# Kernel tuning notes

Measured on AMD Instinct MI355X. Metric: run time of the kernel, lower is better.

## Reference

```python
import jax, jax.numpy as jnp
import numpy as np

RESID = 1024
HEADS = 16
HEAD_DIM = 64


def setup_inputs() -> dict:
    key = jax.random.key(0)
    ks = jax.random.split(key, 6)
    B, S = 2, 2048
    residual_stream = jax.random.normal(ks[0], (B, S, RESID), dtype=jnp.float32)
    # per-head qkv linear params, stacked over heads: [H, resid, 3*head_dim]
    W_qkv = jax.random.normal(ks[1], (HEADS, RESID, 3 * HEAD_DIM), dtype=jnp.float32) * (1.0 / np.sqrt(RESID))
    b_qkv = jax.random.normal(ks[2], (HEADS, 3 * HEAD_DIM), dtype=jnp.float32) * 0.01
    # output projection resid -> resid
    W_o = jax.random.normal(ks[3], (RESID, RESID), dtype=jnp.float32) * (1.0 / np.sqrt(RESID))
    b_o = jax.random.normal(ks[4], (RESID,), dtype=jnp.float32) * 0.01
    return {"residual_stream": residual_stream, "W_qkv": W_qkv, "b_qkv": b_qkv, "W_o": W_o, "b_o": b_o}


def reference(residual_stream, W_qkv, b_qkv, W_o, b_o):
    # qkv per head: [B, H, S, 3*D]
    qkv = jnp.einsum('bsr,hrd->bhsd', residual_stream, W_qkv) + b_qkv[None, :, None, :]
    q = qkv[..., :HEAD_DIM]
    k = qkv[..., HEAD_DIM:2 * HEAD_DIM]
    v = qkv[..., 2 * HEAD_DIM:]
    # NOTE: original has no causal mask; softmax over full key axis
    scores = jnp.einsum('bhsd,bhtd->bhst', q, k) / jnp.sqrt(jnp.float32(HEAD_DIM))
    attn = jax.nn.softmax(scores, axis=-1)
    out = jnp.einsum('bhst,bhtd->bhsd', attn, v)  # [B, H, S, D]
    B, H, S, D = out.shape
    out = out.transpose(0, 2, 1, 3).reshape(B, S, H * D)  # concat heads -> [B, S, resid]
    return out @ W_o + b_o
```

## Files before the change

kernel.cpp:

```cpp
#include <hip/hip_runtime.h>
#include <hip/hip_bf16.h>

#define B_ 2
#define S_ 2048
#define H_ 16
#define HD 64
#define R_ 1024
#define N_ (B_*S_)

typedef unsigned short ushort_t;
typedef short bf16x8 __attribute__((ext_vector_type(8)));
typedef float f32x4 __attribute__((ext_vector_type(4)));
typedef float f32x16 __attribute__((ext_vector_type(16)));

#define MFMA(a,b,c) __builtin_amdgcn_mfma_f32_16x16x32_bf16(a,b,c,0,0,0)
#define MFMA32(a,b,c) __builtin_amdgcn_mfma_f32_32x32x16_bf16(a,b,c,0,0,0)
#define GLD16(g,l) __builtin_amdgcn_global_load_lds( \
    (const __attribute__((address_space(1))) void*)(g), \
    (__attribute__((address_space(3))) void*)(l), 16, 0, 0)

__device__ __forceinline__ unsigned short f2bf(float f) {
  unsigned int u = __builtin_bit_cast(unsigned int, f);
  u += 0x7fffu + ((u >> 16) & 1u);
  return (unsigned short)(u >> 16);
}

__device__ __forceinline__ unsigned int cvtpk(float lo, float hi) {
  unsigned int r;
  asm("v_cvt_pk_bf16_f32 %0, %1, %2" : "=v"(r) : "v"(lo), "v"(hi));
  return r;
}

__device__ __forceinline__ void plswap(unsigned int &a, unsigned int &b) {
  asm volatile("v_permlane32_swap_b32 %0, %1" : "+v"(a), "+v"(b));
}

#if __has_builtin(__builtin_amdgcn_exp2f)
__device__ __forceinline__ float EXP2(float x) { return __builtin_amdgcn_exp2f(x); }
#else
__device__ __forceinline__ float EXP2(float x) {
  float r; asm("v_exp_f32 %0, %1" : "=v"(r) : "v"(x)); return r;
}
#endif

#if __has_builtin(__builtin_amdgcn_rcpf)
__device__ __forceinline__ float RCP(float x) { return __builtin_amdgcn_rcpf(x); }
#else
__device__ __forceinline__ float RCP(float x) { return 1.0f / x; }
#endif

__device__ __forceinline__ bf16x8 ld8(const ushort_t* p) {
  return *(const bf16x8*)p;
}

__device__ __forceinline__ void transpose_tile(const float* __restrict__ in,
                                               ushort_t* __restrict__ out,
                                               int rows, int cols, int rt, int ct,
                                               float (*t)[65], int tid) {
  const int r0 = rt * 64, c0 = ct * 64;
  const int tx = tid & 63, ty = tid >> 6;
  #pragma unroll
  for (int i = 0; i < 16; i++) {
    int r = ty * 16 + i;
    t[r][tx] = in[(size_t)(r0 + r) * cols + c0 + tx];
  }
  __syncthreads();
  #pragma unroll
  for (int i = 0; i < 16; i++) {
    int c = ty * 16 + i;
    out[(size_t)(c0 + c) * rows + r0 + tx] = f2bf(t[tx][c]);
  }
}

__global__ __launch_bounds__(256) void k_prep(
    const float* __restrict__ x, ushort_t* __restrict__ xb,
    const float* __restrict__ Wqkv, ushort_t* __restrict__ WT,
    const float* __restrict__ Wo, ushort_t* __restrict__ WoT) {
  __shared__ float t[64][65];
  const int bid = blockIdx.x, tid = threadIdx.x;
  if (bid < 4096) {
    int i = bid * 256 + tid;
    float4 v = ((const float4*)x)[i];
    ushort4 o;
    o.x = f2bf(v.x); o.y = f2bf(v.y); o.z = f2bf(v.z); o.w = f2bf(v.w);
    ((ushort4*)xb)[i] = o;
  } else if (bid < 4096 + 768) {
    int tt = bid - 4096;
    int z = tt / 48, rem = tt % 48;
    transpose_tile(Wqkv + (size_t)z * 1024 * 192, WT + (size_t)z * 192 * 1024,
                   1024, 192, rem % 16, rem / 16, t, tid);
  } else {
    int tt = bid - (4096 + 768);
    transpose_tile(Wo, WoT, 1024, 1024, tt % 16, tt / 16, t, tid);
  }
}

__global__ __launch_bounds__(256, 2) void k_qkv(
    const ushort_t* __restrict__ Xb, const ushort_t* __restrict__ WT,
    const float* __restrict__ bqkv,
    ushort_t* __restrict__ Q, ushort_t* __restrict__ K, ushort_t* __restrict__ Vt) {
  __shared__ ushort_t lA[2][128 * 32];
  __shared__ ushort_t lB[2][192 * 32];
  const int m0 = blockIdx.x * 128;
  const int h  = blockIdx.y;
  const int tid = threadIdx.x;
  const int w = tid >> 6, l = tid & 63;
  const int lr = l & 15, lg = l >> 4;
  const int wr = w >> 1, wc = w & 1;

  const ushort_t* Asrc = Xb + (size_t)m0 * R_;
  const ushort_t* Bsrc = WT + (size_t)h * 192 * R_;
  const int arow = l >> 2;
  const int acol = (l & 3) * 8;

  f32x4 acc[4][6];
  const f32x4 fz = {0.f, 0.f, 0.f, 0.f};
  #pragma unroll
  for (int m = 0; m < 4; m++)
    #pragma unroll
    for (int n = 0; n < 6; n++) acc[m][n] = fz;

  auto stage = [&](int buf, int kt) {
    const int k0 = kt * 32;
    #pragma unroll
    for (int i = 0; i < 2; i++) {
      int chunk = w + 4 * i;
      GLD16(Asrc + (size_t)(chunk * 16 + arow) * R_ + k0 + acol, &lA[buf][chunk * 512]);
    }
    #pragma unroll
    for (int i = 0; i < 3; i++) {
      int chunk = w + 4 * i;
      GLD16(Bsrc + (size_t)(chunk * 16 + arow) * R_ + k0 + acol, &lB[buf][chunk * 512]);
    }
  };

  stage(0, 0);
  asm volatile("s_waitcnt vmcnt(0)" ::: "memory");
  __syncthreads();

  int cur = 0;
  for (int kt = 0; kt < 32; ++kt) {
    if (kt < 31) stage(cur ^ 1, kt + 1);
    bf16x8 af[4], bfr[6];
    #pragma unroll
    for (int m = 0; m < 4; m++)
      af[m] = ld8(&lA[cur][(wr * 64 + m * 16 + lr) * 32 + lg * 8]);
    #pragma unroll
    for (int n = 0; n < 6; n++)
      bfr[n] = ld8(&lB[cur][(wc * 96 + n * 16 + lr) * 32 + lg * 8]);
    __builtin_amdgcn_s_setprio(1);
    #pragma unroll
    for (int m = 0; m < 4; m++)
      #pragma unroll
      for (int n = 0; n < 6; n++)
        acc[m][n] = MFMA(af[m], bfr[n], acc[m][n]);
    __builtin_amdgcn_s_setprio(0);
    asm volatile("s_waitcnt vmcnt(0)" ::: "memory");
    __syncthreads();
    cur ^= 1;
  }

  #pragma unroll
  for (int n = 0; n < 6; n++) {
    const int col = wc * 96 + n * 16 + lr;
    const float bias = bqkv[h * 192 + col];
    #pragma unroll
    for (int m = 0; m < 4; m++) {
      const int rb = m0 + wr * 64 + m * 16 + lg * 4;
      #pragma unroll
      for (int r = 0; r < 4; r++) {
        float v = acc[m][n][r] + bias;
        int srow = rb + r;
        int b = srow >> 11, s = srow & 2047;
        size_t bh = (size_t)b * H_ + h;
        if (col < 64) {
          Q[(bh * S_ + s) * HD + col] = f2bf(v * 0.1803368801111137f);
        } else if (col < 128) {
          int d = col - 64;
          K[(bh * S_ + s) * HD + d] = f2bf(v);
        } else {
          int d = col - 128;
          Vt[(bh * HD + d) * S_ + s] = f2bf(v);
        }
      }
    }
  }
}

__global__ __launch_bounds__(256, 2) void k_attn(
    const ushort_t* __restrict__ Q, const ushort_t* __restrict__ K,
    const ushort_t* __restrict__ Vt, ushort_t* __restrict__ AO) {
  __shared__ ushort_t sK[3][64 * 64];
  __shared__ ushort_t sV[3][64 * 64];
  const int qt = blockIdx.x;
  const int bh = blockIdx.y;
  const int b = bh >> 4, h = bh & 15;
  const int tid = threadIdx.x, w = tid >> 6, l = tid & 63;
  const int lq = l & 31, hi = l >> 5;

  const ushort_t* Qb = Q + (size_t)bh * S_ * HD;
  const ushort_t* Kb = K + (size_t)bh * S_ * HD;
  const ushort_t* Vb = Vt + (size_t)bh * HD * S_;

  bf16x8 qf[4];
  {
    int qrow = qt * 128 + 32 * w + lq;
    #pragma unroll
    for (int kd = 0; kd < 4; kd++)
      qf[kd] = ld8(&Qb[(size_t)qrow * HD + kd * 16 + hi * 8]);
  }

  const int sr = l >> 3;
  const int scol = l & 7;
  const int r0l = w * 16 + sr;
  const ushort_t* kp = Kb + (size_t)r0l * HD + scol * 8;
  const ushort_t* vp = Vb + (size_t)r0l * S_ + scol * 8;
  bf16x8 kreg0, kreg1, vreg0, vreg1;
  int tnext = 0;
  auto issue = [&]() {
    if (tnext < 32) {
      kreg0 = ld8(kp); kreg1 = ld8(kp + 8 * HD);
      vreg0 = ld8(vp); vreg1 = ld8(vp + 8 * S_);
      kp += 64 * HD; vp += 64;
    }
    ++tnext;
  };
  const int coff0 = r0l * 64 + ((scol ^ sr) * 8);
  const int coff1 = coff0 + 8 * 64;
  auto commit = [&](ushort_t* bK, ushort_t* bV) {
    *(bf16x8*)&bK[coff0] = kreg0; *(bf16x8*)&bK[coff1] = kreg1;
    *(bf16x8*)&bV[coff0] = vreg0; *(bf16x8*)&bV[coff1] = vreg1;
  };

  const f32x16 fz16 = {0};
  const bf16x8 onesv = {0x3F80, 0x3F80, 0x3F80, 0x3F80, 0x3F80, 0x3F80, 0x3F80, 0x3F80};
  f32x16 oacc0 = fz16, oacc1 = fz16, ssv = fz16;

  const int c = hi ^ (lq & 7);

  auto QK = [&](const ushort_t* bK, f32x16& s0, f32x16& s1) {
    f32x16 a0 = fz16, a1 = fz16;
    __builtin_amdgcn_s_setprio(1);
    #pragma unroll
    for (int kd = 0; kd < 4; kd++) {
      const int sl = ((kd * 2) ^ c) * 8;
      bf16x8 ka0 = ld8(&bK[lq * 64 + sl]);
      bf16x8 ka1 = ld8(&bK[(32 + lq) * 64 + sl]);
      a0 = MFMA32(ka0, qf[kd], a0);
      a1 = MFMA32(ka1, qf[kd], a1);
    }
    __builtin_amdgcn_s_setprio(0);
    s0 = a0; s1 = a1;
  };

  auto SMPV = [&](const ushort_t* bV, f32x16 s0, f32x16 s1) {
    #pragma unroll
    for (int n = 0; n < 2; n++) {
      const f32x16 scv = n ? s1 : s0;
      float e[16];
      #pragma unroll
      for (int r = 0; r < 16; r++) e[r] = EXP2(scv[r]);
      #pragma unroll
      for (int sl2 = 0; sl2 < 2; sl2++) {
        unsigned int X  = cvtpk(e[8 * sl2 + 0], e[8 * sl2 + 1]);
        unsigned int Y  = cvtpk(e[8 * sl2 + 2], e[8 * sl2 + 3]);
        unsigned int X2 = cvtpk(e[8 * sl2 + 4], e[8 * sl2 + 5]);
        unsigned int Y2 = cvtpk(e[8 * sl2 + 6], e[8 * sl2 + 7]);
        plswap(X, X2);
        plswap(Y, Y2);
        int4 wv = {(int)X, (int)Y, (int)X2, (int)Y2};
        bf16x8 pa = __builtin_bit_cast(bf16x8, wv);
        const int ks = n * 2 + sl2;
        const int sl3 = ((ks * 2) ^ c) * 8;
        __builtin_amdgcn_s_setprio(1);
        ssv = MFMA32(pa, onesv, ssv);
        {
          bf16x8 vb0 = ld8(&bV[lq * 64 + sl3]);
          bf16x8 vb1 = ld8(&bV[(32 + lq) * 64 + sl3]);
          oacc0 = MFMA32(pa, vb0, oacc0);
          oacc1 = MFMA32(pa, vb1, oacc1);
        }
        __builtin_amdgcn_s_setprio(0);
      }
    }
  };

  f32x16 scA0, scA1, scB0, scB1;
  issue();
  commit(sK[0], sV[0]);
  issue();
  __syncthreads();
  QK(sK[0], scA0, scA1);
  commit(sK[1], sV[1]);
  __syncthreads();
  issue();

#define ABODY(C, N, O, SI0, SI1, SO0, SO1) \
    QK(sK[N], SO0, SO1); \
    SMPV(sV[C], SI0, SI1); \
    commit(sK[O], sV[O]); \
    issue(); \
    __syncthreads();

  for (int kt = 0; kt < 30; kt += 6) {
    ABODY(0, 1, 2, scA0, scA1, scB0, scB1)
    ABODY(1, 2, 0, scB0, scB1, scA0, scA1)
    ABODY(2, 0, 1, scA0, scA1, scB0, scB1)
    ABODY(0, 1, 2, scB0, scB1, scA0, scA1)
    ABODY(1, 2, 0, scA0, scA1, scB0, scB1)
    ABODY(2, 0, 1, scB0, scB1, scA0, scA1)
  }
#undef ABODY

  QK(sK[1], scB0, scB1);
  SMPV(sV[0], scA0, scA1);
  SMPV(sV[1], scB0, scB1);

  #pragma unroll
  for (int reg = 0; reg < 16; reg++) {
    float inv = RCP(ssv[reg]);
    int qloc = (reg & 3) + 8 * (reg >> 2) + 4 * hi;
    int s = qt * 128 + 32 * w + qloc;
    AO[(size_t)(b * S_ + s) * R_ + h * HD + lq] = f2bf(oacc0[reg] * inv);
    AO[(size_t)(b * S_ + s) * R_ + h * HD + 32 + lq] = f2bf(oacc1[reg] * inv);
  }
}

__global__ __launch_bounds__(256, 2) void k_out(
    const ushort_t* __restrict__ AO, const ushort_t* __restrict__ WoT,
    const float* __restrict__ bo, float* __restrict__ out) {
  __shared__ ushort_t lA[2][128 * 32];
  __shared__ ushort_t lB[2][128 * 32];
  const int m0 = blockIdx.x * 128, n0 = blockIdx.y * 128;
  const int tid = threadIdx.x, w = tid >> 6, l = tid & 63;
  const int lr = l & 15, lg = l >> 4;
  const int wr = w >> 1, wc = w & 1;
  const ushort_t* Asrc = AO + (size_t)m0 * R_;
  const ushort_t* Bsrc = WoT + (size_t)n0 * R_;
  const int arow = l >> 2, acol = (l & 3) * 8;

  f32x4 acc[4][4];
  const f32x4 fz = {0.f, 0.f, 0.f, 0.f};
  #pragma unroll
  for (int m = 0; m < 4; m++)
    #pragma unroll
    for (int n = 0; n < 4; n++) acc[m][n] = fz;

  auto stage = [&](int buf, int kt) {
    const int k0 = kt * 32;
    #pragma unroll
    for (int i = 0; i < 2; i++) {
      int chunk = w + 4 * i;
      GLD16(Asrc + (size_t)(chunk * 16 + arow) * R_ + k0 + acol, &lA[buf][chunk * 512]);
      GLD16(Bsrc + (size_t)(chunk * 16 + arow) * R_ + k0 + acol, &lB[buf][chunk * 512]);
    }
  };

  stage(0, 0);
  asm volatile("s_waitcnt vmcnt(0)" ::: "memory");
  __syncthreads();

  int cur = 0;
  for (int kt = 0; kt < 32; ++kt) {
    if (kt < 31) stage(cur ^ 1, kt + 1);
    bf16x8 af[4], bfr[4];
    #pragma unroll
    for (int m = 0; m < 4; m++)
      af[m] = ld8(&lA[cur][(wr * 64 + m * 16 + lr) * 32 + lg * 8]);
    #pragma unroll
    for (int n = 0; n < 4; n++)
      bfr[n] = ld8(&lB[cur][(wc * 64 + n * 16 + lr) * 32 + lg * 8]);
    __builtin_amdgcn_s_setprio(1);
    #pragma unroll
    for (int m = 0; m < 4; m++)
      #pragma unroll
      for (int n = 0; n < 4; n++)
        acc[m][n] = MFMA(af[m], bfr[n], acc[m][n]);
    __builtin_amdgcn_s_setprio(0);
    asm volatile("s_waitcnt vmcnt(0)" ::: "memory");
    __syncthreads();
    cur ^= 1;
  }

  #pragma unroll
  for (int n = 0; n < 4; n++) {
    const int col = n0 + wc * 64 + n * 16 + lr;
    const float bias = bo[col];
    #pragma unroll
    for (int m = 0; m < 4; m++) {
      const int row = m0 + wr * 64 + m * 16 + lg * 4;
      #pragma unroll
      for (int r = 0; r < 4; r++)
        out[(size_t)(row + r) * R_ + col] = acc[m][n][r] + bias;
    }
  }
}

extern "C" void kernel_launch(void* const* d_in, const int* in_sizes, int n_in,
                              void* d_out, int out_size, void* d_ws, size_t ws_size,
                              hipStream_t stream) {
  const float* resid = (const float*)d_in[0];
  const float* Wqkv  = (const float*)d_in[1];
  const float* bqkv  = (const float*)d_in[2];
  const float* Wo    = (const float*)d_in[3];
  const float* bo    = (const float*)d_in[4];
  float* out = (float*)d_out;

  ushort_t* Xb  = (ushort_t*)d_ws;
  ushort_t* WT  = Xb  + (size_t)N_ * R_;
  ushort_t* WoT = WT  + (size_t)H_ * 192 * R_;
  ushort_t* Qd  = WoT + (size_t)R_ * R_;
  ushort_t* Kd  = Qd  + (size_t)B_ * H_ * S_ * HD;
  ushort_t* Vtd = Kd  + (size_t)B_ * H_ * S_ * HD;
  ushort_t* AOd = Vtd + (size_t)B_ * H_ * S_ * HD;

  k_prep<<<dim3(4096 + 768 + 256), dim3(256), 0, stream>>>(resid, Xb, Wqkv, WT, Wo, WoT);
  k_qkv<<<dim3(32, 16), dim3(256), 0, stream>>>(Xb, WT, bqkv, Qd, Kd, Vtd);
  k_attn<<<dim3(16, 32), dim3(256), 0, stream>>>(Qd, Kd, Vtd, AOd);
  k_out<<<dim3(32, 8), dim3(256), 0, stream>>>(AOd, WoT, bo, out);
}
```

Before: 120.2 us.

## Retile QKV GEMM to 128x128 across heads and XOR-swizzle LDS in GEMMs

```diff
diff --git a/kernel.cpp b/kernel.cpp
--- a/kernel.cpp
+++ b/kernel.cpp
@@ -95,30 +95,30 @@
   }
 }
 
-__global__ __launch_bounds__(256, 2) void k_qkv(
+__global__ __launch_bounds__(256, 3) void k_qkv(
     const ushort_t* __restrict__ Xb, const ushort_t* __restrict__ WT,
     const float* __restrict__ bqkv,
     ushort_t* __restrict__ Q, ushort_t* __restrict__ K, ushort_t* __restrict__ Vt) {
   __shared__ ushort_t lA[2][128 * 32];
-  __shared__ ushort_t lB[2][192 * 32];
+  __shared__ ushort_t lB[2][128 * 32];
   const int m0 = blockIdx.x * 128;
-  const int h  = blockIdx.y;
+  const int n0 = blockIdx.y * 128;
   const int tid = threadIdx.x;
   const int w = tid >> 6, l = tid & 63;
   const int lr = l & 15, lg = l >> 4;
   const int wr = w >> 1, wc = w & 1;
 
   const ushort_t* Asrc = Xb + (size_t)m0 * R_;
-  const ushort_t* Bsrc = WT + (size_t)h * 192 * R_;
+  const ushort_t* Bsrc = WT + (size_t)n0 * R_;
   const int arow = l >> 2;
-  const int acol = (l & 3) * 8;
-
-  f32x4 acc[4][6];
+  const int acol = ((l & 3) ^ ((arow >> 1) & 3)) * 8;
+
+  f32x4 acc[4][4];
   const f32x4 fz = {0.f, 0.f, 0.f, 0.f};
   #pragma unroll
   for (int m = 0; m < 4; m++)
     #pragma unroll
-    for (int n = 0; n < 6; n++) acc[m][n] = fz;
+    for (int n = 0; n < 4; n++) acc[m][n] = fz;
 
   auto stage = [&](int buf, int kt) {
     const int k0 = kt * 32;
@@ -126,10 +126,6 @@
     for (int i = 0; i < 2; i++) {
       int chunk = w + 4 * i;
       GLD16(Asrc + (size_t)(chunk * 16 + arow) * R_ + k0 + acol, &lA[buf][chunk * 512]);
-    }
-    #pragma unroll
-    for (int i = 0; i < 3; i++) {
-      int chunk = w + 4 * i;
       GLD16(Bsrc + (size_t)(chunk * 16 + arow) * R_ + k0 + acol, &lB[buf][chunk * 512]);
     }
   };
@@ -138,21 +134,22 @@
   asm volatile("s_waitcnt vmcnt(0)" ::: "memory");
   __syncthreads();
 
+  const int rsw = (lr >> 1) & 3;
   int cur = 0;
   for (int kt = 0; kt < 32; ++kt) {
     if (kt < 31) stage(cur ^ 1, kt + 1);
-    bf16x8 af[4], bfr[6];
+    bf16x8 af[4], bfr[4];
     #pragma unroll
     for (int m = 0; m < 4; m++)
-      af[m] = ld8(&lA[cur][(wr * 64 + m * 16 + lr) * 32 + lg * 8]);
-    #pragma unroll
-    for (int n = 0; n < 6; n++)
-      bfr[n] = ld8(&lB[cur][(wc * 96 + n * 16 + lr) * 32 + lg * 8]);
+      af[m] = ld8(&lA[cur][(wr * 64 + m * 16 + lr) * 32 + ((lg ^ rsw) * 8)]);
+    #pragma unroll
+    for (int n = 0; n < 4; n++)
+      bfr[n] = ld8(&lB[cur][(wc * 64 + n * 16 + lr) * 32 + ((lg ^ rsw) * 8)]);
     __builtin_amdgcn_s_setprio(1);
     #pragma unroll
     for (int m = 0; m < 4; m++)
       #pragma unroll
-      for (int n = 0; n < 6; n++)
+      for (int n = 0; n < 4; n++)
         acc[m][n] = MFMA(af[m], bfr[n], acc[m][n]);
     __builtin_amdgcn_s_setprio(0);
     asm volatile("s_waitcnt vmcnt(0)" ::: "memory");
@@ -161,9 +158,11 @@
   }
 
   #pragma unroll
-  for (int n = 0; n < 6; n++) {
-    const int col = wc * 96 + n * 16 + lr;
-    const float bias = bqkv[h * 192 + col];
+  for (int n = 0; n < 4; n++) {
+    const int col = n0 + wc * 64 + n * 16 + lr;
+    const int h = col / 192;
+    const int cc = col - h * 192;
+    const float bias = bqkv[col];
     #pragma unroll
     for (int m = 0; m < 4; m++) {
       const int rb = m0 + wr * 64 + m * 16 + lg * 4;
@@ -173,13 +172,13 @@
         int srow = rb + r;
         int b = srow >> 11, s = srow & 2047;
         size_t bh = (size_t)b * H_ + h;
-        if (col < 64) {
-          Q[(bh * S_ + s) * HD + col] = f2bf(v * 0.1803368801111137f);
-        } else if (col < 128) {
-          int d = col - 64;
+        if (cc < 64) {
+          Q[(bh * S_ + s) * HD + cc] = f2bf(v * 0.1803368801111137f);
+        } else if (cc < 128) {
+          int d = cc - 64;
           K[(bh * S_ + s) * HD + d] = f2bf(v);
         } else {
-          int d = col - 128;
+          int d = cc - 128;
           Vt[(bh * HD + d) * S_ + s] = f2bf(v);
         }
       }
@@ -337,7 +336,8 @@
   const int wr = w >> 1, wc = w & 1;
   const ushort_t* Asrc = AO + (size_t)m0 * R_;
   const ushort_t* Bsrc = WoT + (size_t)n0 * R_;
-  const int arow = l >> 2, acol = (l & 3) * 8;
+  const int arow = l >> 2;
+  const int acol = ((l & 3) ^ ((arow >> 1) & 3)) * 8;
 
   f32x4 acc[4][4];
   const f32x4 fz = {0.f, 0.f, 0.f, 0.f};
@@ -360,16 +360,17 @@
   asm volatile("s_waitcnt vmcnt(0)" ::: "memory");
   __syncthreads();
 
+  const int rsw = (lr >> 1) & 3;
   int cur = 0;
   for (int kt = 0; kt < 32; ++kt) {
     if (kt < 31) stage(cur ^ 1, kt + 1);
     bf16x8 af[4], bfr[4];
     #pragma unroll
     for (int m = 0; m < 4; m++)
-      af[m] = ld8(&lA[cur][(wr * 64 + m * 16 + lr) * 32 + lg * 8]);
+      af[m] = ld8(&lA[cur][(wr * 64 + m * 16 + lr) * 32 + ((lg ^ rsw) * 8)]);
     #pragma unroll
     for (int n = 0; n < 4; n++)
-      bfr[n] = ld8(&lB[cur][(wc * 64 + n * 16 + lr) * 32 + lg * 8]);
+      bfr[n] = ld8(&lB[cur][(wc * 64 + n * 16 + lr) * 32 + ((lg ^ rsw) * 8)]);
     __builtin_amdgcn_s_setprio(1);
     #pragma unroll
     for (int m = 0; m < 4; m++)
@@ -415,7 +416,7 @@
   ushort_t* AOd = Vtd + (size_t)B_ * H_ * S_ * HD;
 
   k_prep<<<dim3(4096 + 768 + 256), dim3(256), 0, stream>>>(resid, Xb, Wqkv, WT, Wo, WoT);
-  k_qkv<<<dim3(32, 16), dim3(256), 0, stream>>>(Xb, WT, bqkv, Qd, Kd, Vtd);
+  k_qkv<<<dim3(32, 24), dim3(256), 0, stream>>>(Xb, WT, bqkv, Qd, Kd, Vtd);
   k_attn<<<dim3(16, 32), dim3(256), 0, stream>>>(Qd, Kd, Vtd, AOd);
   k_out<<<dim3(32, 8), dim3(256), 0, stream>>>(AOd, WoT, bo, out);
 }
```

Result: faster. 117.7 us (-2.1%).
